# Kernel optimization log

Measured on AMD Instinct MI355X. Metric: run time of the kernel, lower is better.

## Reference

```python
import jax, jax.numpy as jnp
import numpy as np

DN = ('NCHW', 'OIHW', 'NCHW')

def conv3x3(x, w):
    return jax.lax.conv_general_dilated(x, w, (1, 1), [(1, 1), (1, 1)], dimension_numbers=DN)

def setup_inputs() -> dict:
    key = jax.random.key(0)
    ks = jax.random.split(key, 5)
    N, C, H, W = 64, 512, 16, 16
    fan = C * 3 * 3
    s = 1.0 / np.sqrt(fan)
    x = jax.random.normal(ks[0], (N, C, H, W), dtype=jnp.float32)
    Wq = jax.random.normal(ks[1], (C, C, 3, 3), dtype=jnp.float32) * s
    Wk = jax.random.normal(ks[2], (C, C, 3, 3), dtype=jnp.float32) * s
    Wv = jax.random.normal(ks[3], (C, C, 3, 3), dtype=jnp.float32) * s
    Wc = jax.random.normal(ks[4], (C, C, 3, 3), dtype=jnp.float32) * s
    gamma = jnp.ones((C,), dtype=jnp.float32)
    beta = jnp.zeros((C,), dtype=jnp.float32)
    return {"x": x, "Wq": Wq, "Wk": Wk, "Wv": Wv, "Wc": Wc, "gamma": gamma, "beta": beta}

def reference(x, Wq, Wk, Wv, Wc, gamma, beta):
    C = x.shape[1]
    q = conv3x3(x, Wq)  # [N,C,H,W]
    k = conv3x3(x, Wk)
    v = conv3x3(x, Wv)
    # att[n,m,h,w] = sum_c q[n,c,h,w] * k[m,c,h,w] / sqrt(C); softmax over m
    att = jnp.einsum('nchw,mchw->nmhw', q, k) / jnp.sqrt(jnp.float32(C))
    att = jax.nn.softmax(att, axis=1)
    # virt[n,c,h,w] = sum_m att[n,m,h,w] * v[m,c,h,w]
    virt = jnp.einsum('nmhw,mchw->nchw', att, v)
    # GroupNorm(1, C): normalize over (C,H,W) per sample, per-channel affine
    mu = jnp.mean(virt, axis=(1, 2, 3), keepdims=True)
    var = jnp.var(virt, axis=(1, 2, 3), keepdims=True)
    virt = (virt - mu) * jax.lax.rsqrt(var + 1e-5)
    virt = virt * gamma[None, :, None, None] + beta[None, :, None, None]
    virt = jax.nn.relu(virt)
    virt = conv3x3(virt, Wc)
    # Dropout is identity in eval mode
    return x + virt
```

## Files before the change

kernel.cpp:

```cpp
#include <hip/hip_runtime.h>
#include <math.h>

typedef unsigned short u16;
typedef unsigned int u32;
typedef short short8 __attribute__((ext_vector_type(8)));
typedef float f32x4 __attribute__((ext_vector_type(4)));

#define NB 64
#define CCH 512
#define HW 256

__device__ __forceinline__ u16 f2bf(float f) {
    union { float f; u32 u; } x; x.f = f;
    u32 r = x.u + 0x7fffu + ((x.u >> 16) & 1u);
    return (u16)(r >> 16);
}
__device__ __forceinline__ float bf2f(u16 b) {
    union { u32 u; float f; } x; x.u = ((u32)b) << 16;
    return x.f;
}
__device__ __forceinline__ void gload_lds16(const u16* g, u16* l) {
    __builtin_amdgcn_global_load_lds((const __attribute__((address_space(1))) u32*)g,
                                     (__attribute__((address_space(3))) u32*)l, 16, 0, 0);
}

__global__ __launch_bounds__(256) void zero_borders(u16* __restrict__ pad) {
    const int n = blockIdx.x, t = threadIdx.x;
    short8 z = (short8){0,0,0,0,0,0,0,0};
    for (int idx = t; idx < 68 * 64; idx += 256) {
        int cell = idx >> 6, ch = idx & 63;
        int hh, ww;
        if (cell < 18)      { hh = 0;          ww = cell; }
        else if (cell < 36) { hh = 17;         ww = cell - 18; }
        else if (cell < 52) { hh = cell - 35;  ww = 0; }
        else                { hh = cell - 51;  ww = 17; }
        *(short8*)(pad + ((size_t)((n * 18 + hh) * 18 + ww)) * 512 + ch * 8) = z;
    }
}

__global__ __launch_bounds__(256) void prep_x(const float* __restrict__ x, u16* __restrict__ pad) {
    __shared__ float tl[64][65];
    const int n = blockIdx.z, c0 = blockIdx.y * 64, p0 = blockIdx.x * 64;
    const int t = threadIdx.x;
    {
        const int cc = t >> 2, ps = (t & 3) * 16;
#pragma unroll
        for (int i = 0; i < 4; ++i) {
            float4 v4 = *(const float4*)(x + (((size_t)(n * 512 + c0 + cc)) << 8) + p0 + ps + i * 4);
            tl[cc][ps + i * 4 + 0] = v4.x;
            tl[cc][ps + i * 4 + 1] = v4.y;
            tl[cc][ps + i * 4 + 2] = v4.z;
            tl[cc][ps + i * 4 + 3] = v4.w;
        }
    }
    __syncthreads();
    {
        const int pp = t >> 2, cs = (t & 3) * 16;
        short8 o0, o1;
#pragma unroll
        for (int i = 0; i < 8; ++i) o0[i] = (short)f2bf(tl[cs + i][pp]);
#pragma unroll
        for (int i = 0; i < 8; ++i) o1[i] = (short)f2bf(tl[cs + 8 + i][pp]);
        const int p = p0 + pp, h = p >> 4, wcol = p & 15;
        u16* dst = pad + ((size_t)((n * 18 + h + 1) * 18 + wcol + 1)) * 512 + c0 + cs;
        *(short8*)(dst + 0) = o0;
        *(short8*)(dst + 8) = o1;
    }
}

__global__ __launch_bounds__(256) void prep_w(
    const float* __restrict__ Wq, const float* __restrict__ Wk,
    const float* __restrict__ Wv, const float* __restrict__ Wc,
    u16* __restrict__ Wt)
{
    __shared__ float lw[4608];
    const int co = blockIdx.x, sel = blockIdx.y, t = threadIdx.x;
    const float* Ws = (sel == 0) ? Wq : (sel == 1) ? Wk : (sel == 2) ? Wv : Wc;
#pragma unroll
    for (int i = 0; i < 18; ++i) lw[t + i * 256] = Ws[(size_t)co * 4608 + t + i * 256];
    __syncthreads();
    for (int tap = 0; tap < 9; ++tap)
#pragma unroll
        for (int hh = 0; hh < 2; ++hh) {
            int ci = t + hh * 256;
            Wt[(((size_t)(sel * 9 + tap)) << 18) + (co << 9) + ci] = f2bf(lw[ci * 9 + tap]);
        }
}

__global__ __launch_bounds__(512, 1) void qkv_mfma8(
    const u16* __restrict__ pad, const u16* __restrict__ Wt,
    u16* __restrict__ q, u16* __restrict__ k, u16* __restrict__ v)
{
    __shared__ short As[3][8192];
    __shared__ short Bs[3][6144];
    const int t = threadIdx.x;
    const int l = t & 63;
    const int wid = t >> 6;
    const int wm = wid >> 2, wn = wid & 3;

    const int o = blockIdx.x;
    const int wg = (o & 7) * 64 + (o >> 3);
    const int imbase = (wg >> 3) * 256;
    const int cobase = (wg & 7) * 192;

    const int cl = ((l & 3) - ((l >> 3) & 3)) & 3;
    int imoffA[2], woffB[2];
#pragma unroll
    for (int rr = 0; rr < 2; ++rr) {
        const int chunk = wid * 2 + rr;
        const int imrow = imbase + chunk * 16 + (l >> 2);
        const int p = imrow >> 6, n = imrow & 63;
        imoffA[rr] = ((n * 18 + (p >> 4)) * 18 + (p & 15)) * 512 + cl * 8;
        const int cof = cobase + chunk * 16 + (l >> 2);
        const int sel = cof >> 9, co = cof & 511;
        woffB[rr] = sel * 9 * 262144 + co * 512 + cl * 8;
    }

    const int fp = ((l >> 4) + (l >> 1)) & 3;
    const int aoff = (wm * 128 + (l & 15)) * 32 + fp * 8;
    const int boff = (wn * 48 + (l & 15)) * 32 + fp * 8;

    f32x4 acc[8][3];
#pragma unroll
    for (int i = 0; i < 8; ++i)
#pragma unroll
        for (int j = 0; j < 3; ++j) acc[i][j] = (f32x4){0.f, 0.f, 0.f, 0.f};

    auto STAGE_A = [&](int kt, int s) {
        const int tap = kt >> 4;
        const int shift = ((tap / 3) * 18 + (tap % 3)) * 512 + (kt & 15) * 32;
#pragma unroll
        for (int rr = 0; rr < 2; ++rr)
            gload_lds16(pad + imoffA[rr] + shift, (u16*)(&As[s][0] + (wid * 2 + rr) * 512));
    };
    auto STAGE_B = [&](int kt, int s) {
        if (wid < 6) {
            const int tap = kt >> 4;
            const int shift = tap * 262144 + (kt & 15) * 32;
#pragma unroll
            for (int rr = 0; rr < 2; ++rr)
                gload_lds16(Wt + woffB[rr] + shift, (u16*)(&Bs[s][0] + (wid * 2 + rr) * 512));
        }
    };

    STAGE_A(0, 0); STAGE_B(0, 0);
    STAGE_A(1, 1); STAGE_B(1, 1);

    int s0 = 0;
    short8 fa[8], fb[3];
#pragma unroll 1
    for (int kt = 0; kt < 144; ++kt) {
        const int s2 = (s0 == 0) ? 2 : s0 - 1;
        const short* Ab = &As[s0][0];
        const short* Bb = &Bs[s0][0];

        if (kt >= 143) {
            asm volatile("s_waitcnt vmcnt(0)" ::: "memory");
        } else if (wid < 6) {
            asm volatile("s_waitcnt vmcnt(4)" ::: "memory");
        } else {
            asm volatile("s_waitcnt vmcnt(2)" ::: "memory");
        }
        __builtin_amdgcn_sched_barrier(0);
        __builtin_amdgcn_s_barrier();
        __builtin_amdgcn_sched_barrier(0);

#pragma unroll
        for (int j = 0; j < 3; ++j) fb[j] = *(const short8*)(Bb + boff + j * 512);
#pragma unroll
        for (int i = 0; i < 8; ++i) fa[i] = *(const short8*)(Ab + aoff + i * 512);

        if (kt < 142) { STAGE_A(kt + 2, s2); STAGE_B(kt + 2, s2); }

        __builtin_amdgcn_s_setprio(1);
#pragma unroll
        for (int i = 0; i < 8; ++i)
#pragma unroll
            for (int j = 0; j < 3; ++j)
                acc[i][j] = __builtin_amdgcn_mfma_f32_16x16x32_bf16(fa[i], fb[j], acc[i][j], 0, 0, 0);
        __builtin_amdgcn_s_setprio(0);

        s0 = (s0 == 2) ? 0 : s0 + 1;
    }

#pragma unroll
    for (int j = 0; j < 3; ++j) {
        const int colb = cobase + wn * 48 + j * 16;
        u16* op = ((colb >> 9) == 0) ? q : (((colb >> 9) == 1) ? k : v);
        op += (colb & 511) + (l & 15);
#pragma unroll
        for (int i = 0; i < 8; ++i) {
            const int row = imbase + wm * 128 + i * 16 + (l >> 4) * 4;
#pragma unroll
            for (int r = 0; r < 4; ++r)
                op[(size_t)(row + r) * 512] = f2bf(acc[i][j][r]);
        }
    }
}

__global__ __launch_bounds__(256, 2) void cres_mfma4(
    const u16* __restrict__ pad, const u16* __restrict__ WtC,
    const float* __restrict__ xres, float* __restrict__ out)
{
    __shared__ short As[3][4096];
    __shared__ short Bs[3][4096];
    const int t = threadIdx.x;
    const int l = t & 63;
    const int wid = t >> 6;
    const int wm = wid >> 1, wn = wid & 1;

    const int o = blockIdx.x;
    const int cobase = (o & 3) * 128;
    const int imbase = (o >> 2) * 128;

    const int cl = ((l & 3) - ((l >> 3) & 3)) & 3;
    int woffA[2], imoffB[2];
#pragma unroll
    for (int rr = 0; rr < 2; ++rr) {
        const int co = cobase + (wid * 2 + rr) * 16 + (l >> 2);
        woffA[rr] = co * 512 + cl * 8;
        const int imrow = imbase + (wid * 2 + rr) * 16 + (l >> 2);
        const int n = imrow >> 8, p = imrow & 255;
        imoffB[rr] = ((n * 18 + (p >> 4)) * 18 + (p & 15)) * 512 + cl * 8;
    }

    const int fp = ((l >> 4) + (l >> 1)) & 3;
    const int aoff = (wm * 64 + (l & 15)) * 32 + fp * 8;
    const int boff = (wn * 64 + (l & 15)) * 32 + fp * 8;

    f32x4 acc[4][4];
#pragma unroll
    for (int i = 0; i < 4; ++i)
#pragma unroll
        for (int j = 0; j < 4; ++j) acc[i][j] = (f32x4){0.f, 0.f, 0.f, 0.f};

    auto STAGE = [&](int kt, int s) {
        const int tap = kt >> 4;
        const int ashift = tap * 262144 + (kt & 15) * 32;
        const int bshift = ((tap / 3) * 18 + (tap % 3)) * 512 + (kt & 15) * 32;
#pragma unroll
        for (int rr = 0; rr < 2; ++rr) {
            gload_lds16(WtC + woffA[rr] + ashift, (u16*)(&As[s][0] + (wid * 2 + rr) * 512));
            gload_lds16(pad + imoffB[rr] + bshift, (u16*)(&Bs[s][0] + (wid * 2 + rr) * 512));
        }
    };

    STAGE(0, 0);
    STAGE(1, 1);

    int s0 = 0;
    short8 fa[4], fb[4];
#pragma unroll 1
    for (int kt = 0; kt < 144; ++kt) {
        const int s2 = (s0 == 0) ? 2 : s0 - 1;
        const short* Ab = &As[s0][0];
        const short* Bb = &Bs[s0][0];

        if (kt >= 143) asm volatile("s_waitcnt vmcnt(0)" ::: "memory");
        else           asm volatile("s_waitcnt vmcnt(4)" ::: "memory");
        __builtin_amdgcn_sched_barrier(0);
        __builtin_amdgcn_s_barrier();
        __builtin_amdgcn_sched_barrier(0);

#pragma unroll
        for (int i = 0; i < 4; ++i) fa[i] = *(const short8*)(Ab + aoff + i * 512);
#pragma unroll
        for (int j = 0; j < 4; ++j) fb[j] = *(const short8*)(Bb + boff + j * 512);

        if (kt < 142) STAGE(kt + 2, s2);

        __builtin_amdgcn_s_setprio(1);
#pragma unroll
        for (int i = 0; i < 4; ++i)
#pragma unroll
            for (int j = 0; j < 4; ++j)
                acc[i][j] = __builtin_amdgcn_mfma_f32_16x16x32_bf16(fa[i], fb[j], acc[i][j], 0, 0, 0);
        __builtin_amdgcn_s_setprio(0);

        s0 = (s0 == 2) ? 0 : s0 + 1;
    }

#pragma unroll
    for (int i = 0; i < 4; ++i)
#pragma unroll
        for (int j = 0; j < 4; ++j)
#pragma unroll
            for (int r = 0; r < 4; ++r) {
                int co = cobase + wm * 64 + i * 16 + (l >> 4) * 4 + r;
                int imrow = imbase + wn * 64 + j * 16 + (l & 15);
                int n = imrow >> 8, p = imrow & 255;
                size_t addr = (((size_t)(n * 512 + co)) << 8) + p;
                out[addr] = acc[i][j][r] + xres[addr];
            }
}

__global__ __launch_bounds__(256) void attn_kernel(
    const u16* __restrict__ qT, const u16* __restrict__ kT, u16* vvT,
    float* __restrict__ gnp)
{
    const int p = blockIdx.x;
    const int t = threadIdx.x;
    const int l = t & 63;
    const int w = t >> 6;
    __shared__ float attb[64][68];
    __shared__ float vs[8448];
    const size_t pb = (size_t)p * (NB * CCH);

    const u16* qbase = qT + pb + (size_t)(w * 16 + (l & 15)) * 512 + (l >> 4) * 8;
    const u16* kbase = kT + pb + (size_t)(l & 15) * 512 + (l >> 4) * 8;
    f32x4 s[4];
#pragma unroll
    for (int j = 0; j < 4; ++j) s[j] = (f32x4){0.f, 0.f, 0.f, 0.f};
#pragma unroll 4
    for (int kc = 0; kc < 16; ++kc) {
        short8 a = *(const short8*)(qbase + kc * 32);
#pragma unroll
        for (int j = 0; j < 4; ++j) {
            short8 b = *(const short8*)(kbase + (size_t)j * 16 * 512 + kc * 32);
            s[j] = __builtin_amdgcn_mfma_f32_16x16x32_bf16(a, b, s[j], 0, 0, 0);
        }
    }

    const float SCALE = 0.0441941738241592f;
#pragma unroll
    for (int r = 0; r < 4; ++r) {
        float mx = fmaxf(fmaxf(s[0][r], s[1][r]), fmaxf(s[2][r], s[3][r]));
#pragma unroll
        for (int mask = 1; mask < 16; mask <<= 1) mx = fmaxf(mx, __shfl_xor(mx, mask));
        float e[4]; float sm = 0.f;
#pragma unroll
        for (int j = 0; j < 4; ++j) { e[j] = __expf((s[j][r] - mx) * SCALE); sm += e[j]; }
#pragma unroll
        for (int mask = 1; mask < 16; mask <<= 1) sm += __shfl_xor(sm, mask);
        float inv = 1.f / sm;
        const int row = w * 16 + (l >> 4) * 4 + r;
#pragma unroll
        for (int j = 0; j < 4; ++j) attb[row][j * 16 + (l & 15)] = e[j] * inv;
    }
    __syncthreads();

    const int ng2 = t >> 3, cg = t & 7;
    const int nn0 = ng2 * 2, cb = cg * 16;
    float rsum[2] = {0.f, 0.f}, rss[2] = {0.f, 0.f};
    for (int ct4 = 0; ct4 < 4; ++ct4) {
        const int c0 = ct4 * 128;
#pragma unroll
        for (int sld = 0; sld < 4; ++sld) {
            int f = t + sld * 256;
            int m = f >> 4, c8 = (f & 15) * 8;
            short8 vv = *(const short8*)(vvT + pb + (size_t)m * CCH + c0 + c8);
#pragma unroll
            for (int e = 0; e < 8; ++e) vs[m * 132 + c8 + e] = bf2f((u16)vv[e]);
        }
        __syncthreads();
        float acc2[2][16];
#pragma unroll
        for (int i = 0; i < 2; ++i)
#pragma unroll
            for (int j = 0; j < 16; ++j) acc2[i][j] = 0.f;
#pragma unroll 4
        for (int m = 0; m < 64; ++m) {
            float a0 = attb[nn0][m], a1 = attb[nn0 + 1][m];
#pragma unroll
            for (int k4 = 0; k4 < 4; ++k4) {
                float4 v4 = *(const float4*)&vs[m * 132 + cb + k4 * 4];
                acc2[0][k4 * 4 + 0] = fmaf(a0, v4.x, acc2[0][k4 * 4 + 0]);
                acc2[0][k4 * 4 + 1] = fmaf(a0, v4.y, acc2[0][k4 * 4 + 1]);
                acc2[0][k4 * 4 + 2] = fmaf(a0, v4.z, acc2[0][k4 * 4 + 2]);
                acc2[0][k4 * 4 + 3] = fmaf(a0, v4.w, acc2[0][k4 * 4 + 3]);
                acc2[1][k4 * 4 + 0] = fmaf(a1, v4.x, acc2[1][k4 * 4 + 0]);
                acc2[1][k4 * 4 + 1] = fmaf(a1, v4.y, acc2[1][k4 * 4 + 1]);
                acc2[1][k4 * 4 + 2] = fmaf(a1, v4.z, acc2[1][k4 * 4 + 2]);
                acc2[1][k4 * 4 + 3] = fmaf(a1, v4.w, acc2[1][k4 * 4 + 3]);
            }
        }
#pragma unroll
        for (int i = 0; i < 2; ++i)
#pragma unroll
            for (int j = 0; j < 16; ++j) {
                float x = acc2[i][j];
                rsum[i] += x;
                rss[i] = fmaf(x, x, rss[i]);
                vvT[pb + (size_t)(nn0 + i) * CCH + c0 + cb + j] = f2bf(x);
            }
        __syncthreads();
    }

#pragma unroll
    for (int i = 0; i < 2; ++i) {
#pragma unroll
        for (int mask = 1; mask < 8; mask <<= 1) {
            rsum[i] += __shfl_xor(rsum[i], mask);
            rss[i]  += __shfl_xor(rss[i],  mask);
        }
    }
    if (cg == 0) {
#pragma unroll
        for (int i = 0; i < 2; ++i) {
            gnp[((size_t)p * 64 + nn0 + i) * 2 + 0] = rsum[i];
            gnp[((size_t)p * 64 + nn0 + i) * 2 + 1] = rss[i];
        }
    }
}

__global__ __launch_bounds__(256) void gn_part2(
    const u16* __restrict__ virtT, const float* __restrict__ gnp,
    const float* __restrict__ gamma, const float* __restrict__ beta,
    u16* __restrict__ ypad)
{
    const int n = blockIdx.x >> 2, qr = blockIdx.x & 3, t = threadIdx.x;
    __shared__ float sg[512], sb[512];
    for (int i = t; i < 512; i += 256) { sg[i] = gamma[i]; sb[i] = beta[i]; }

    float sum = gnp[((size_t)t * 64 + n) * 2 + 0];
    float ss  = gnp[((size_t)t * 64 + n) * 2 + 1];
#pragma unroll
    for (int off = 32; off > 0; off >>= 1) {
        sum += __shfl_down(sum, off);
        ss  += __shfl_down(ss, off);
    }
    __shared__ float rs[4], rss[4], stats[2];
    const int wid = t >> 6, lane = t & 63;
    if (lane == 0) { rs[wid] = sum; rss[wid] = ss; }
    __syncthreads();
    if (t == 0) {
        float S = rs[0] + rs[1] + rs[2] + rs[3];
        float SS = rss[0] + rss[1] + rss[2] + rss[3];
        float mu = S * (1.f / 131072.f);
        float var = SS * (1.f / 131072.f) - mu * mu;
        stats[0] = mu;
        stats[1] = rsqrtf(var + 1e-5f);
    }
    __syncthreads();
    const float mu = stats[0], rstd = stats[1];

#pragma unroll 4
    for (int it = 0; it < 16; ++it) {
        int f = t + it * 256;
        int p = qr * 64 + (f >> 6), cc = (f & 63) * 8;
        short8 vv = *(const short8*)(virtT + ((size_t)(p * 64 + n)) * 512 + cc);
        short8 ov;
#pragma unroll
        for (int e = 0; e < 8; ++e) {
            float x = (bf2f((u16)vv[e]) - mu) * rstd;
            x = fmaf(x, sg[cc + e], sb[cc + e]);
            ov[e] = (short)f2bf(fmaxf(x, 0.f));
        }
        int h = p >> 4, wcol = p & 15;
        *(short8*)(ypad + ((size_t)((n * 18 + h + 1) * 18 + wcol + 1)) * 512 + cc) = ov;
    }
}

extern "C" void kernel_launch(void* const* d_in, const int* in_sizes, int n_in,
                              void* d_out, int out_size, void* d_ws, size_t ws_size,
                              hipStream_t stream)
{
    const float* x     = (const float*)d_in[0];
    const float* Wq    = (const float*)d_in[1];
    const float* Wk    = (const float*)d_in[2];
    const float* Wv    = (const float*)d_in[3];
    const float* Wc    = (const float*)d_in[4];
    const float* gamma = (const float*)d_in[5];
    const float* beta  = (const float*)d_in[6];
    float* out = (float*)d_out;

    u16* pad = (u16*)d_ws;
    u16* Wt  = pad + 10616832;
    u16* q   = Wt + 9437184;
    u16* k   = q + 8388608;
    u16* v   = k + 8388608;
    float* gnp = (float*)Wt;

    zero_borders<<<dim3(64), dim3(256), 0, stream>>>(pad);
    prep_x<<<dim3(4, 8, 64), dim3(256), 0, stream>>>(x, pad);
    prep_w<<<dim3(512, 4), dim3(256), 0, stream>>>(Wq, Wk, Wv, Wc, Wt);

    qkv_mfma8<<<dim3(512), dim3(512), 0, stream>>>(pad, Wt, q, k, v);
    attn_kernel<<<dim3(256), dim3(256), 0, stream>>>(q, k, v, gnp);
    gn_part2<<<dim3(256), dim3(256), 0, stream>>>(v, gnp, gamma, beta, pad);
    cres_mfma4<<<dim3(512), dim3(256), 0, stream>>>(pad, Wt + 3 * 2359296, x, out);
}
```

Measured before the change: 391.0 us.

## Widen QKV conv GEMM tile to 256x384 and stream A fragments

```diff
diff --git a/kernel.cpp b/kernel.cpp
--- a/kernel.cpp
+++ b/kernel.cpp
@@ -87,105 +87,98 @@
         }
 }
 
-__global__ __launch_bounds__(512, 1) void qkv_mfma8(
+__global__ __launch_bounds__(512) void qkv_wide(
     const u16* __restrict__ pad, const u16* __restrict__ Wt,
     u16* __restrict__ q, u16* __restrict__ k, u16* __restrict__ v)
 {
     __shared__ short As[3][8192];
-    __shared__ short Bs[3][6144];
+    __shared__ short Bs[3][12288];
     const int t = threadIdx.x;
     const int l = t & 63;
     const int wid = t >> 6;
     const int wm = wid >> 2, wn = wid & 3;
 
     const int o = blockIdx.x;
-    const int wg = (o & 7) * 64 + (o >> 3);
-    const int imbase = (wg >> 3) * 256;
-    const int cobase = (wg & 7) * 192;
+    const int wg = (o & 7) * 32 + (o >> 3);
+    const int imbase = (wg >> 2) * 256;
+    const int cobase = (wg & 3) * 384;
 
     const int cl = ((l & 3) - ((l >> 3) & 3)) & 3;
-    int imoffA[2], woffB[2];
+    int imoffA[2], woffB[3];
 #pragma unroll
     for (int rr = 0; rr < 2; ++rr) {
         const int chunk = wid * 2 + rr;
         const int imrow = imbase + chunk * 16 + (l >> 2);
         const int p = imrow >> 6, n = imrow & 63;
         imoffA[rr] = ((n * 18 + (p >> 4)) * 18 + (p & 15)) * 512 + cl * 8;
-        const int cof = cobase + chunk * 16 + (l >> 2);
+    }
+#pragma unroll
+    for (int rr = 0; rr < 3; ++rr) {
+        const int cof = cobase + (wid * 3 + rr) * 16 + (l >> 2);
         const int sel = cof >> 9, co = cof & 511;
         woffB[rr] = sel * 9 * 262144 + co * 512 + cl * 8;
     }
 
     const int fp = ((l >> 4) + (l >> 1)) & 3;
     const int aoff = (wm * 128 + (l & 15)) * 32 + fp * 8;
-    const int boff = (wn * 48 + (l & 15)) * 32 + fp * 8;
-
-    f32x4 acc[8][3];
+    const int boff = (wn * 96 + (l & 15)) * 32 + fp * 8;
+
+    f32x4 acc[8][6];
 #pragma unroll
     for (int i = 0; i < 8; ++i)
 #pragma unroll
-        for (int j = 0; j < 3; ++j) acc[i][j] = (f32x4){0.f, 0.f, 0.f, 0.f};
-
-    auto STAGE_A = [&](int kt, int s) {
+        for (int j = 0; j < 6; ++j) acc[i][j] = (f32x4){0.f, 0.f, 0.f, 0.f};
+
+    auto STAGE = [&](int kt, int s) {
         const int tap = kt >> 4;
-        const int shift = ((tap / 3) * 18 + (tap % 3)) * 512 + (kt & 15) * 32;
+        const int ashift = ((tap / 3) * 18 + (tap % 3)) * 512 + (kt & 15) * 32;
+        const int bshift = tap * 262144 + (kt & 15) * 32;
 #pragma unroll
         for (int rr = 0; rr < 2; ++rr)
-            gload_lds16(pad + imoffA[rr] + shift, (u16*)(&As[s][0] + (wid * 2 + rr) * 512));
+            gload_lds16(pad + imoffA[rr] + ashift, (u16*)(&As[s][0] + (wid * 2 + rr) * 512));
+#pragma unroll
+        for (int rr = 0; rr < 3; ++rr)
+            gload_lds16(Wt + woffB[rr] + bshift, (u16*)(&Bs[s][0] + (wid * 3 + rr) * 512));
     };
-    auto STAGE_B = [&](int kt, int s) {
-        if (wid < 6) {
-            const int tap = kt >> 4;
-            const int shift = tap * 262144 + (kt & 15) * 32;
-#pragma unroll
-            for (int rr = 0; rr < 2; ++rr)
-                gload_lds16(Wt + woffB[rr] + shift, (u16*)(&Bs[s][0] + (wid * 2 + rr) * 512));
-        }
-    };
-
-    STAGE_A(0, 0); STAGE_B(0, 0);
-    STAGE_A(1, 1); STAGE_B(1, 1);
+
+    STAGE(0, 0);
+    STAGE(1, 1);
 
     int s0 = 0;
-    short8 fa[8], fb[3];
+    short8 fb[6];
 #pragma unroll 1
     for (int kt = 0; kt < 144; ++kt) {
         const int s2 = (s0 == 0) ? 2 : s0 - 1;
         const short* Ab = &As[s0][0];
         const short* Bb = &Bs[s0][0];
 
-        if (kt >= 143) {
-            asm volatile("s_waitcnt vmcnt(0)" ::: "memory");
-        } else if (wid < 6) {
-            asm volatile("s_waitcnt vmcnt(4)" ::: "memory");
-        } else {
-            asm volatile("s_waitcnt vmcnt(2)" ::: "memory");
-        }
+        if (kt >= 143) asm volatile("s_waitcnt vmcnt(0)" ::: "memory");
+        else           asm volatile("s_waitcnt vmcnt(5)" ::: "memory");
         __builtin_amdgcn_sched_barrier(0);
         __builtin_amdgcn_s_barrier();
         __builtin_amdgcn_sched_barrier(0);
 
 #pragma unroll
-        for (int j = 0; j < 3; ++j) fb[j] = *(const short8*)(Bb + boff + j * 512);
-#pragma unroll
-        for (int i = 0; i < 8; ++i) fa[i] = *(const short8*)(Ab + aoff + i * 512);
-
-        if (kt < 142) { STAGE_A(kt + 2, s2); STAGE_B(kt + 2, s2); }
+        for (int j = 0; j < 6; ++j) fb[j] = *(const short8*)(Bb + boff + j * 512);
+
+        if (kt < 142) STAGE(kt + 2, s2);
 
         __builtin_amdgcn_s_setprio(1);
 #pragma unroll
-        for (int i = 0; i < 8; ++i)
-#pragma unroll
-            for (int j = 0; j < 3; ++j)
-                acc[i][j] = __builtin_amdgcn_mfma_f32_16x16x32_bf16(fa[i], fb[j], acc[i][j], 0, 0, 0);
+        for (int i = 0; i < 8; ++i) {
+            short8 fa = *(const short8*)(Ab + aoff + i * 512);
+#pragma unroll
+            for (int j = 0; j < 6; ++j)
+                acc[i][j] = __builtin_amdgcn_mfma_f32_16x16x32_bf16(fa, fb[j], acc[i][j], 0, 0, 0);
+        }
         __builtin_amdgcn_s_setprio(0);
 
         s0 = (s0 == 2) ? 0 : s0 + 1;
     }
 
 #pragma unroll
-    for (int j = 0; j < 3; ++j) {
-        const int colb = cobase + wn * 48 + j * 16;
+    for (int j = 0; j < 6; ++j) {
+        const int colb = cobase + wn * 96 + j * 16;
         u16* op = ((colb >> 9) == 0) ? q : (((colb >> 9) == 1) ? k : v);
         op += (colb & 511) + (l & 15);
 #pragma unroll
@@ -475,7 +468,7 @@
     prep_x<<<dim3(4, 8, 64), dim3(256), 0, stream>>>(x, pad);
     prep_w<<<dim3(512, 4), dim3(256), 0, stream>>>(Wq, Wk, Wv, Wc, Wt);
 
-    qkv_mfma8<<<dim3(512), dim3(512), 0, stream>>>(pad, Wt, q, k, v);
+    qkv_wide<<<dim3(256), dim3(512), 0, stream>>>(pad, Wt, q, k, v);
     attn_kernel<<<dim3(256), dim3(256), 0, stream>>>(q, k, v, gnp);
     gn_part2<<<dim3(256), dim3(256), 0, stream>>>(v, gnp, gamma, beta, pad);
     cres_mfma4<<<dim3(512), dim3(256), 0, stream>>>(pad, Wt + 3 * 2359296, x, out);
```

New measurement: 393.2 us. No clear change (+0.6%).

## Use MFMA for attention-times-V with transposed V layout from QKV epilogue

Applied to the files above, without the earlier changes.

```diff
diff --git a/kernel.cpp b/kernel.cpp
--- a/kernel.cpp
+++ b/kernel.cpp
@@ -4,6 +4,7 @@
 typedef unsigned short u16;
 typedef unsigned int u32;
 typedef short short8 __attribute__((ext_vector_type(8)));
+typedef short short4v __attribute__((ext_vector_type(4)));
 typedef float f32x4 __attribute__((ext_vector_type(4)));
 
 #define NB 64
@@ -186,14 +187,28 @@
 #pragma unroll
     for (int j = 0; j < 3; ++j) {
         const int colb = cobase + wn * 48 + j * 16;
-        u16* op = ((colb >> 9) == 0) ? q : (((colb >> 9) == 1) ? k : v);
-        op += (colb & 511) + (l & 15);
-#pragma unroll
-        for (int i = 0; i < 8; ++i) {
-            const int row = imbase + wm * 128 + i * 16 + (l >> 4) * 4;
-#pragma unroll
-            for (int r = 0; r < 4; ++r)
-                op[(size_t)(row + r) * 512] = f2bf(acc[i][j][r]);
+        const int sel = colb >> 9;
+        if (sel == 2) {
+            const int c = (colb & 511) + (l & 15);
+#pragma unroll
+            for (int i = 0; i < 8; ++i) {
+                const int rowb = imbase + wm * 128 + i * 16 + (l >> 4) * 4;
+                const int pp = rowb >> 6, nb = rowb & 63;
+                short4v sv;
+#pragma unroll
+                for (int r = 0; r < 4; ++r) sv[r] = (short)f2bf(acc[i][j][r]);
+                *(short4v*)(v + (size_t)pp * 32768 + (size_t)c * 64 + nb) = sv;
+            }
+        } else {
+            u16* op = (sel == 0) ? q : k;
+            op += (colb & 511) + (l & 15);
+#pragma unroll
+            for (int i = 0; i < 8; ++i) {
+                const int row = imbase + wm * 128 + i * 16 + (l >> 4) * 4;
+#pragma unroll
+                for (int r = 0; r < 4; ++r)
+                    op[(size_t)(row + r) * 512] = f2bf(acc[i][j][r]);
+            }
         }
     }
 }
@@ -295,15 +310,15 @@
 }
 
 __global__ __launch_bounds__(256) void attn_kernel(
-    const u16* __restrict__ qT, const u16* __restrict__ kT, u16* vvT,
+    u16* __restrict__ qT, const u16* __restrict__ kT, const u16* __restrict__ vT2,
     float* __restrict__ gnp)
 {
     const int p = blockIdx.x;
     const int t = threadIdx.x;
     const int l = t & 63;
     const int w = t >> 6;
-    __shared__ float attb[64][68];
-    __shared__ float vs[8448];
+    __shared__ u16 attB[64][72];
+    __shared__ float gnw_s[4][64], gnw_q[4][64];
     const size_t pb = (size_t)p * (NB * CCH);
 
     const u16* qbase = qT + pb + (size_t)(w * 16 + (l & 15)) * 512 + (l >> 4) * 8;
@@ -335,71 +350,63 @@
         float inv = 1.f / sm;
         const int row = w * 16 + (l >> 4) * 4 + r;
 #pragma unroll
-        for (int j = 0; j < 4; ++j) attb[row][j * 16 + (l & 15)] = e[j] * inv;
-    }
-    __syncthreads();
-
-    const int ng2 = t >> 3, cg = t & 7;
-    const int nn0 = ng2 * 2, cb = cg * 16;
-    float rsum[2] = {0.f, 0.f}, rss[2] = {0.f, 0.f};
-    for (int ct4 = 0; ct4 < 4; ++ct4) {
-        const int c0 = ct4 * 128;
-#pragma unroll
-        for (int sld = 0; sld < 4; ++sld) {
-            int f = t + sld * 256;
-            int m = f >> 4, c8 = (f & 15) * 8;
-            short8 vv = *(const short8*)(vvT + pb + (size_t)m * CCH + c0 + c8);
-#pragma unroll
-            for (int e = 0; e < 8; ++e) vs[m * 132 + c8 + e] = bf2f((u16)vv[e]);
-        }
-        __syncthreads();
-        float acc2[2][16];
-#pragma unroll
-        for (int i = 0; i < 2; ++i)
-#pragma unroll
-            for (int j = 0; j < 16; ++j) acc2[i][j] = 0.f;
-#pragma unroll 4
-        for (int m = 0; m < 64; ++m) {
-            float a0 = attb[nn0][m], a1 = attb[nn0 + 1][m];
-#pragma unroll
-            for (int k4 = 0; k4 < 4; ++k4) {
-                float4 v4 = *(const float4*)&vs[m * 132 + cb + k4 * 4];
-                acc2[0][k4 * 4 + 0] = fmaf(a0, v4.x, acc2[0][k4 * 4 + 0]);
-                acc2[0][k4 * 4 + 1] = fmaf(a0, v4.y, acc2[0][k4 * 4 + 1]);
-                acc2[0][k4 * 4 + 2] = fmaf(a0, v4.z, acc2[0][k4 * 4 + 2]);
-                acc2[0][k4 * 4 + 3] = fmaf(a0, v4.w, acc2[0][k4 * 4 + 3]);
-                acc2[1][k4 * 4 + 0] = fmaf(a1, v4.x, acc2[1][k4 * 4 + 0]);
-                acc2[1][k4 * 4 + 1] = fmaf(a1, v4.y, acc2[1][k4 * 4 + 1]);
-                acc2[1][k4 * 4 + 2] = fmaf(a1, v4.z, acc2[1][k4 * 4 + 2]);
-                acc2[1][k4 * 4 + 3] = fmaf(a1, v4.w, acc2[1][k4 * 4 + 3]);
-            }
-        }
-#pragma unroll
-        for (int i = 0; i < 2; ++i)
-#pragma unroll
-            for (int j = 0; j < 16; ++j) {
-                float x = acc2[i][j];
-                rsum[i] += x;
-                rss[i] = fmaf(x, x, rss[i]);
-                vvT[pb + (size_t)(nn0 + i) * CCH + c0 + cb + j] = f2bf(x);
-            }
-        __syncthreads();
-    }
-
-#pragma unroll
-    for (int i = 0; i < 2; ++i) {
-#pragma unroll
-        for (int mask = 1; mask < 8; mask <<= 1) {
-            rsum[i] += __shfl_xor(rsum[i], mask);
-            rss[i]  += __shfl_xor(rss[i],  mask);
-        }
-    }
-    if (cg == 0) {
-#pragma unroll
-        for (int i = 0; i < 2; ++i) {
-            gnp[((size_t)p * 64 + nn0 + i) * 2 + 0] = rsum[i];
-            gnp[((size_t)p * 64 + nn0 + i) * 2 + 1] = rss[i];
-        }
+        for (int j = 0; j < 4; ++j) attB[row][j * 16 + (l & 15)] = f2bf(e[j] * inv);
+    }
+    __syncthreads();
+
+    const int cb = w * 128;
+    const u16* vb = vT2 + (size_t)p * 32768 + (size_t)(cb + (l & 15)) * 64 + (l >> 4) * 8;
+
+#pragma unroll 1
+    for (int nt = 0; nt < 4; ++nt) {
+        short8 fa0 = *(const short8*)(&attB[nt * 16 + (l & 15)][(l >> 4) * 8]);
+        short8 fa1 = *(const short8*)(&attB[nt * 16 + (l & 15)][(l >> 4) * 8 + 32]);
+        f32x4 acc[8];
+#pragma unroll
+        for (int ct = 0; ct < 8; ++ct) acc[ct] = (f32x4){0.f, 0.f, 0.f, 0.f};
+#pragma unroll
+        for (int ct = 0; ct < 8; ++ct) {
+            short8 fb0 = *(const short8*)(vb + ct * 1024);
+            short8 fb1 = *(const short8*)(vb + ct * 1024 + 32);
+            acc[ct] = __builtin_amdgcn_mfma_f32_16x16x32_bf16(fa0, fb0, acc[ct], 0, 0, 0);
+            acc[ct] = __builtin_amdgcn_mfma_f32_16x16x32_bf16(fa1, fb1, acc[ct], 0, 0, 0);
+        }
+        float ps[4] = {0.f, 0.f, 0.f, 0.f}, pq[4] = {0.f, 0.f, 0.f, 0.f};
+#pragma unroll
+        for (int ct = 0; ct < 8; ++ct) {
+            const int c = cb + ct * 16 + (l & 15);
+#pragma unroll
+            for (int r = 0; r < 4; ++r) {
+                float x = acc[ct][r];
+                ps[r] += x;
+                pq[r] = fmaf(x, x, pq[r]);
+                const int n = nt * 16 + (l >> 4) * 4 + r;
+                qT[pb + (size_t)n * 512 + c] = f2bf(x);
+            }
+        }
+#pragma unroll
+        for (int r = 0; r < 4; ++r) {
+#pragma unroll
+            for (int mask = 1; mask < 16; mask <<= 1) {
+                ps[r] += __shfl_xor(ps[r], mask);
+                pq[r] += __shfl_xor(pq[r], mask);
+            }
+        }
+        if ((l & 15) == 0) {
+#pragma unroll
+            for (int r = 0; r < 4; ++r) {
+                const int n = nt * 16 + (l >> 4) * 4 + r;
+                gnw_s[w][n] = ps[r];
+                gnw_q[w][n] = pq[r];
+            }
+        }
+    }
+    __syncthreads();
+    if (t < 64) {
+        float S = gnw_s[0][t] + gnw_s[1][t] + gnw_s[2][t] + gnw_s[3][t];
+        float Q = gnw_q[0][t] + gnw_q[1][t] + gnw_q[2][t] + gnw_q[3][t];
+        gnp[((size_t)p * 64 + t) * 2 + 0] = S;
+        gnp[((size_t)p * 64 + t) * 2 + 1] = Q;
     }
 }
 
@@ -477,6 +484,6 @@
 
     qkv_mfma8<<<dim3(512), dim3(512), 0, stream>>>(pad, Wt, q, k, v);
     attn_kernel<<<dim3(256), dim3(256), 0, stream>>>(q, k, v, gnp);
-    gn_part2<<<dim3(256), dim3(256), 0, stream>>>(v, gnp, gamma, beta, pad);
+    gn_part2<<<dim3(256), dim3(256), 0, stream>>>(q, gnp, gamma, beta, pad);
     cres_mfma4<<<dim3(512), dim3(256), 0, stream>>>(pad, Wt + 3 * 2359296, x, out);
 }
```

Result: faster. 369.4 us (-5.5%).
